# Performance work log

Hardware: AMD Instinct MI355X
Metric: run time of the kernel (lower is better)

Reference implementation:

```python
import jax, jax.numpy as jnp
import numpy as np

DIM = 128
NUM_LAYERS = 2
N_LEGO = 50000
N_POINT = 100000
E_LL = 500000
E_PP = 400000
E_LP = 500000
E_PL = 500000


def _seg_softmax(score, seg, n):
    m = jax.ops.segment_max(score, seg, num_segments=n)
    m = jnp.where(jnp.isfinite(m), m, 0.0)
    e = jnp.exp(score - m[seg])
    d = jax.ops.segment_sum(e, seg, num_segments=n)
    return e / (d[seg] + 1e-16)


def _trans_conv(xs, xd, src, dst, Wq, bq, Wk, bk, Wv, bv, Ws, bs):
    # PyG TransformerConv, heads=1, root skip, no edge features
    q = xd @ Wq + bq
    k = xs @ Wk + bk
    v = xs @ Wv + bv
    score = (q[dst] * k[src]).sum(-1) / jnp.sqrt(jnp.asarray(DIM, q.dtype))
    a = _seg_softmax(score, dst, xd.shape[0])
    agg = jax.ops.segment_sum(a[:, None] * v[src], dst, num_segments=xd.shape[0])
    return agg + xd @ Ws + bs


def _gat_conv(xs, xd, src, dst, W, a_src, a_dst, b):
    # PyG GATConv, heads=1, add_self_loops=False, shared lin for src/dst
    hs = xs @ W
    hd = xd @ W
    score = jax.nn.leaky_relu((hs @ a_src)[src] + (hd @ a_dst)[dst], 0.2)
    a = _seg_softmax(score, dst, xd.shape[0])
    return jax.ops.segment_sum(a[:, None] * hs[src], dst, num_segments=xd.shape[0]) + b


def _edge_conv(x, src, dst, W1, b1, W2, b2):
    # PyG EdgeConv: max_j MLP([x_i, x_j - x_i]); BN treated as identity (eval)
    xi = x[dst]
    h = jax.nn.relu(jnp.concatenate([xi, x[src] - xi], axis=-1) @ W1 + b1)
    m = h @ W2 + b2
    agg = jax.ops.segment_max(m, dst, num_segments=x.shape[0])
    return jnp.where(jnp.isfinite(agg), agg, 0.0)


def _forward(x_lego, x_point, tWq, tbq, tWk, tbk, tWv, tbv, tWs, tbs,
             eW1, eb1, eW2, eb2, gW, gAs, gAd, gb,
             ll_src, ll_dst, pp_src, pp_dst, lp_src, lp_dst, pl_src, pl_dst):
    for layer in range(NUM_LAYERS):
        iA = 2 * layer        # first HeteroConv in the stack
        iB = 2 * layer + 1    # second HeteroConv
        i_lp = 2 * layer      # GAT lego->point instance
        i_pl = 2 * layer + 1  # GAT point->lego instance
        # conv A: 4 relations, HeteroConv sum-aggregation per dst type
        lego_a = _trans_conv(x_lego, x_lego, ll_src, ll_dst,
                             tWq[iA], tbq[iA], tWk[iA], tbk[iA], tWv[iA], tbv[iA], tWs[iA], tbs[iA]) \
               + _gat_conv(x_point, x_lego, pl_src, pl_dst, gW[i_pl], gAs[i_pl], gAd[i_pl], gb[i_pl])
        point_a = _edge_conv(x_point, pp_src, pp_dst, eW1[iA], eb1[iA], eW2[iA], eb2[iA]) \
                + _gat_conv(x_lego, x_point, lp_src, lp_dst, gW[i_lp], gAs[i_lp], gAd[i_lp], gb[i_lp])
        # conv B: intra-type relations only
        x_lego = _trans_conv(lego_a, lego_a, ll_src, ll_dst,
                             tWq[iB], tbq[iB], tWk[iB], tbk[iB], tWv[iB], tbv[iB], tWs[iB], tbs[iB])
        x_point = _edge_conv(point_a, pp_src, pp_dst, eW1[iB], eb1[iB], eW2[iB], eb2[iB])
    return x_lego, x_point


def setup_inputs() -> dict:
    key = jax.random.key(0)
    ks = jax.random.split(key, 32)
    NT = 2 * NUM_LAYERS  # conv instances per conv type
    s = np.float32(1.0 / np.sqrt(DIM))
    sh = np.float32(1.0 / np.sqrt(4 * DIM))
    return {
        "x_lego": jax.random.normal(ks[0], (N_LEGO, DIM), jnp.float32),
        "x_point": jax.random.normal(ks[1], (N_POINT, DIM), jnp.float32),
        "tWq": jax.random.normal(ks[2], (NT, DIM, DIM), jnp.float32) * s,
        "tbq": jnp.zeros((NT, DIM), jnp.float32),
        "tWk": jax.random.normal(ks[3], (NT, DIM, DIM), jnp.float32) * s,
        "tbk": jnp.zeros((NT, DIM), jnp.float32),
        "tWv": jax.random.normal(ks[4], (NT, DIM, DIM), jnp.float32) * s,
        "tbv": jnp.zeros((NT, DIM), jnp.float32),
        "tWs": jax.random.normal(ks[5], (NT, DIM, DIM), jnp.float32) * s,
        "tbs": jnp.zeros((NT, DIM), jnp.float32),
        "eW1": jax.random.normal(ks[6], (NT, 2 * DIM, 4 * DIM), jnp.float32) * s,
        "eb1": jnp.zeros((NT, 4 * DIM), jnp.float32),
        "eW2": jax.random.normal(ks[7], (NT, 4 * DIM, DIM), jnp.float32) * sh,
        "eb2": jnp.zeros((NT, DIM), jnp.float32),
        "gW": jax.random.normal(ks[8], (NT, DIM, DIM), jnp.float32) * s,
        "gAs": jax.random.normal(ks[9], (NT, DIM), jnp.float32) * s,
        "gAd": jax.random.normal(ks[10], (NT, DIM), jnp.float32) * s,
        "gb": jnp.zeros((NT, DIM), jnp.float32),
        "ll_src": jax.random.randint(ks[11], (E_LL,), 0, N_LEGO),
        "ll_dst": jax.random.randint(ks[12], (E_LL,), 0, N_LEGO),
        "pp_src": jax.random.randint(ks[13], (E_PP,), 0, N_POINT),
        "pp_dst": jax.random.randint(ks[14], (E_PP,), 0, N_POINT),
        "lp_src": jax.random.randint(ks[15], (E_LP,), 0, N_LEGO),
        "lp_dst": jax.random.randint(ks[16], (E_LP,), 0, N_POINT),
        "pl_src": jax.random.randint(ks[17], (E_PL,), 0, N_POINT),
        "pl_dst": jax.random.randint(ks[18], (E_PL,), 0, N_LEGO),
    }


def reference(x_lego, x_point, tWq, tbq, tWk, tbk, tWv, tbv, tWs, tbs,
              eW1, eb1, eW2, eb2, gW, gAs, gAd, gb,
              ll_src, ll_dst, pp_src, pp_dst, lp_src, lp_dst, pl_src, pl_dst):
    return _forward(x_lego, x_point, tWq, tbq, tWk, tbk, tWv, tbv, tWs, tbs,
                    eW1, eb1, eW2, eb2, gW, gAs, gAd, gb,
                    ll_src, ll_dst, pp_src, pp_dst, lp_src, lp_dst, pl_src, pl_dst)
```

## Files before the change

### kernel.cpp

```cpp
#include <hip/hip_runtime.h>


typedef unsigned int u32;
typedef unsigned short u16;

#define NL 50000
#define NP 100000
#define ELL 500000
#define EPPE 400000
#define ELPE 500000
#define EPLE 500000
#define ENC_NEG_INF 0x007FFFFFu

using bf16x8 = __attribute__((ext_vector_type(8))) short;
using f32x4  = __attribute__((ext_vector_type(4))) float;
using u16x4  = __attribute__((ext_vector_type(4))) unsigned short;

__device__ __forceinline__ float bf2f(u16 h) { return __uint_as_float(((u32)h) << 16); }
__device__ __forceinline__ u16 f2bf(float f) {
    u32 u = __float_as_uint(f);
    u += 0x7FFFu + ((u >> 16) & 1u);
    return (u16)(u >> 16);
}
__device__ __forceinline__ u32 encf(float f) {
    u32 u = __float_as_uint(f);
    return (u & 0x80000000u) ? ~u : (u | 0x80000000u);
}
__device__ __forceinline__ float decf(u32 u) {
    return __uint_as_float((u & 0x80000000u) ? (u ^ 0x80000000u) : ~u);
}

__global__ void k_detect(const u32* __restrict__ x, u32* __restrict__ flag) {
    int lane = threadIdx.x;
    u16 lo = (u16)(x[lane] & 0xFFFFu);
    float a = fabsf(bf2f(lo));
    int inband = (a > 1e-4f && a < 100.f) ? 1 : 0;
    unsigned long long m = __ballot(inband);
    if (lane == 0) flag[0] = (__popcll(m) >= 32) ? 1u : 0u;
}


__global__ __launch_bounds__(256) void k_cast_any(const void* __restrict__ in,
                                                  float* __restrict__ out, int n,
                                                  const u32* __restrict__ flag) {
    int i = blockIdx.x * 256 + threadIdx.x;
    if (i >= n) return;
    if (flag[0]) out[i] = bf2f(((const u16*)in)[i]);
    else         out[i] = ((const float*)in)[i];
}

__global__ __launch_bounds__(256) void k_store_out(const float* __restrict__ in,
                                                   void* __restrict__ out, size_t off, int n,
                                                   const u32* __restrict__ flag) {
    int i = blockIdx.x * 256 + threadIdx.x;
    if (i >= n) return;
    if (flag[0]) ((u16*)out)[off + i] = f2bf(in[i]);
    else         ((float*)out)[off + i] = in[i];
}

__global__ __launch_bounds__(256) void k_fill_u32(u32* __restrict__ p, u32 v, int n) {
    int i = blockIdx.x * 256 + threadIdx.x;
    if (i < n) p[i] = v;
}

__global__ void k_add128(const float* __restrict__ a, const float* __restrict__ b,
                         float* __restrict__ o) {
    int t = threadIdx.x;
    o[t] = a[t] + b[t];
}

__global__ __launch_bounds__(256) void k_tcast(const float* __restrict__ in,
                                               u16* __restrict__ out,
                                               int K, int N, int total) {
    int i = blockIdx.x * 256 + threadIdx.x;
    if (i >= total) return;
    int per = K * N;
    int c = i / per, r = i - c * per;
    int k = r / N, n = r - k * N;
    out[(size_t)c * per + (size_t)n * K + k] = f2bf(in[i]);
}

__global__ __launch_bounds__(256) void k_w1mod(float* __restrict__ w, int total) {
    int i = blockIdx.x * 256 + threadIdx.x;
    if (i >= total) return;
    int c = i >> 16;
    int r = (i >> 9) & 127;
    int col = i & 511;
    float* base = w + c * 131072;
    base[r * 512 + col] -= base[(r + 128) * 512 + col];
}

__global__ __launch_bounds__(256) void k_split(const float4* __restrict__ x,
                                               u16x4* __restrict__ xh,
                                               u16x4* __restrict__ xl, int n4) {
    int i = blockIdx.x * 256 + threadIdx.x;
    if (i >= n4) return;
    float4 f = x[i];
    float fv[4] = {f.x, f.y, f.z, f.w};
    u16x4 h, l;
#pragma unroll
    for (int j = 0; j < 4; ++j) {
        u16 hi = f2bf(fv[j]);
        h[j] = hi;
        l[j] = f2bf(fv[j] - bf2f(hi));
    }
    xh[i] = h; xl[i] = l;
}

__global__ void k_matvec2(const float* __restrict__ W, const float* __restrict__ a0,
                          const float* __restrict__ a1, float* __restrict__ o) {
    __shared__ float as[128];
    const float* a = blockIdx.x ? a1 : a0;
    int t = threadIdx.x;
    as[t] = a[t];
    __syncthreads();
    float s = 0.f;
#pragma unroll 8
    for (int i = 0; i < 128; ++i) s += W[t * 128 + i] * as[i];
    o[blockIdx.x * 128 + t] = s;
}

__global__ __launch_bounds__(256) void k_node_scalar(const float* __restrict__ X,
                                                     const float* __restrict__ wv,
                                                     float* __restrict__ s, int n) {
    int wid = (blockIdx.x * 256 + threadIdx.x) >> 6;
    int lane = threadIdx.x & 63;
    if (wid >= n) return;
    const float* xr = X + (size_t)wid * 128;
    float v = xr[lane] * wv[lane] + xr[lane + 64] * wv[lane + 64];
#pragma unroll
    for (int o = 32; o; o >>= 1) v += __shfl_xor(v, o);
    if (lane == 0) s[wid] = v;
}


__global__ __launch_bounds__(256) void k_deg(const int* __restrict__ dst,
                                             int* __restrict__ deg, int E) {
    int i = blockIdx.x * 256 + threadIdx.x;
    if (i < E) atomicAdd(deg + dst[i], 1);
}

__global__ __launch_bounds__(256) void k_scan1(const int* __restrict__ deg,
                                               int* __restrict__ rp,
                                               int* __restrict__ aux, int n) {
    __shared__ int ls[256];
    int t = threadIdx.x;
    int i = blockIdx.x * 256 + t;
    int v = (i < n) ? deg[i] : 0;
    ls[t] = v;
    __syncthreads();
#pragma unroll
    for (int off = 1; off < 256; off <<= 1) {
        int a = (t >= off) ? ls[t - off] : 0;
        __syncthreads();
        ls[t] += a;
        __syncthreads();
    }
    if (i < n) rp[i] = ls[t] - v;
    if (t == 255) aux[blockIdx.x] = ls[255];
}

__global__ __launch_bounds__(512) void k_scan2(int* __restrict__ aux, int nb) {
    __shared__ int ls[512];
    int t = threadIdx.x;
    int v = (t < nb) ? aux[t] : 0;
    ls[t] = v;
    __syncthreads();
#pragma unroll
    for (int off = 1; off < 512; off <<= 1) {
        int a = (t >= off) ? ls[t - off] : 0;
        __syncthreads();
        ls[t] += a;
        __syncthreads();
    }
    if (t < nb) aux[t] = ls[t] - v;
}

__global__ __launch_bounds__(256) void k_scan3(int* __restrict__ rp,
                                               const int* __restrict__ aux,
                                               int n, int E) {
    int i = blockIdx.x * 256 + threadIdx.x;
    if (i > n) return;
    if (i == n) rp[n] = E;
    else        rp[i] += aux[i >> 8];
}

__global__ __launch_bounds__(256) void k_copy_i32(const int* __restrict__ a,
                                                  int* __restrict__ b, int n) {
    int i = blockIdx.x * 256 + threadIdx.x;
    if (i < n) b[i] = a[i];
}

__global__ __launch_bounds__(256) void k_scat(const int* __restrict__ src,
                                              const int* __restrict__ dst,
                                              int* __restrict__ cur,
                                              int* __restrict__ col, int E) {
    int i = blockIdx.x * 256 + threadIdx.x;
    if (i >= E) return;
    int pos = atomicAdd(cur + dst[i], 1);
    col[pos] = src[i];
}


__global__ __launch_bounds__(256) void k_attn_trans(const float* __restrict__ Tq,
                                                    const float* __restrict__ Tk,
                                                    const float* __restrict__ Tv,
                                                    const int* __restrict__ rp,
                                                    const int* __restrict__ col,
                                                    float* __restrict__ out, int nd) {
    int row = (blockIdx.x * 256 + threadIdx.x) >> 6;
    int lane = threadIdx.x & 63;
    if (row >= nd) return;
    int e0 = rp[row], e1 = rp[row + 1];
    if (e0 >= e1) return;
    const float* q = Tq + (size_t)row * 128;
    float q0 = q[lane], q1 = q[lane + 64];
    float m = -3.0e38f, l = 0.f, o0 = 0.f, o1 = 0.f;
    for (int e = e0; e < e1; ++e) {
        int s = col[e];
        const float* kr = Tk + (size_t)s * 128;
        float d = q0 * kr[lane] + q1 * kr[lane + 64];
#pragma unroll
        for (int off = 32; off; off >>= 1) d += __shfl_xor(d, off);
        d *= 0.08838834764831845f;
        float mn = fmaxf(m, d);
        float al = expf(m - mn);
        float p  = expf(d - mn);
        const float* vr = Tv + (size_t)s * 128;
        l  = l * al + p;
        o0 = o0 * al + p * vr[lane];
        o1 = o1 * al + p * vr[lane + 64];
        m = mn;
    }
    float inv = 1.f / (l + 1e-16f);
    size_t base = (size_t)row * 128;
    out[base + lane]      += o0 * inv;
    out[base + lane + 64] += o1 * inv;
}

__global__ __launch_bounds__(256) void k_attn_gat(const float* __restrict__ hs,
                                                  const float* __restrict__ ss,
                                                  const float* __restrict__ sd,
                                                  const int* __restrict__ rp,
                                                  const int* __restrict__ col,
                                                  float* __restrict__ out, int nd) {
    int row = (blockIdx.x * 256 + threadIdx.x) >> 6;
    int lane = threadIdx.x & 63;
    if (row >= nd) return;
    int e0 = rp[row], e1 = rp[row + 1];
    if (e0 >= e1) return;
    float sdv = sd[row];
    float m = -3.0e38f, l = 0.f, o0 = 0.f, o1 = 0.f;
    for (int e = e0; e < e1; ++e) {
        int s = col[e];
        float sc = ss[s] + sdv;
        sc = sc > 0.f ? sc : 0.2f * sc;
        float mn = fmaxf(m, sc);
        float al = expf(m - mn);
        float p  = expf(sc - mn);
        const float* hr = hs + (size_t)s * 128;
        l  = l * al + p;
        o0 = o0 * al + p * hr[lane];
        o1 = o1 * al + p * hr[lane + 64];
        m = mn;
    }
    float inv = 1.f / (l + 1e-16f);
    size_t base = (size_t)row * 128;
    out[base + lane]      += o0 * inv;
    out[base + lane + 64] += o1 * inv;
}

#define LSTR 40

__global__ __launch_bounds__(256) void k_mgemm(const float* __restrict__ A_,
                                               const u16* __restrict__ Wt,
                                               const float* __restrict__ bias,
                                               float* __restrict__ Cout,
                                               int M, int N, int K) {
    __shared__ u16 Ahs[128 * LSTR];
    __shared__ u16 Als[128 * LSTR];
    __shared__ u16 Bss[128 * LSTR];
    const int tid = threadIdx.x;
    const int m0 = blockIdx.y * 128, n0 = blockIdx.x * 128;

    const int srow = tid >> 1, sseg = (tid & 1) * 16;
    int arow = m0 + srow;
    if (arow >= M) arow = M - 1;
    const float* Af = A_ + (size_t)arow * K + sseg;
    u16* AhW = &Ahs[srow * LSTR + sseg];
    u16* AlW = &Als[srow * LSTR + sseg];
    const u16* Bp = Wt + (size_t)(n0 + srow) * K + sseg;
    u16* BsW = &Bss[srow * LSTR + sseg];

    const int lane = tid & 63, wv = tid >> 6;
    const int mw = (wv >> 1) * 64, nw = (wv & 1) * 64;
    const int fm = lane & 15, fq = lane >> 4;
    const u16* aRh = &Ahs[(mw + fm) * LSTR + fq * 8];
    const u16* aRl = &Als[(mw + fm) * LSTR + fq * 8];
    const u16* bR  = &Bss[(nw + fm) * LSTR + fq * 8];

    f32x4 acc[4][4];
#pragma unroll
    for (int i = 0; i < 4; ++i)
#pragma unroll
        for (int j = 0; j < 4; ++j) { acc[i][j][0]=0.f; acc[i][j][1]=0.f; acc[i][j][2]=0.f; acc[i][j][3]=0.f; }

    for (int k0 = 0; k0 < K; k0 += 32) {
        __syncthreads();
        float4 f0 = *(const float4*)(Af + k0);
        float4 f1 = *(const float4*)(Af + k0 + 4);
        float4 f2 = *(const float4*)(Af + k0 + 8);
        float4 f3 = *(const float4*)(Af + k0 + 12);
        float v[16] = {f0.x,f0.y,f0.z,f0.w, f1.x,f1.y,f1.z,f1.w,
                       f2.x,f2.y,f2.z,f2.w, f3.x,f3.y,f3.z,f3.w};
        u32 hp[8], lp[8];
#pragma unroll
        for (int i = 0; i < 8; ++i) {
            float x0 = v[2 * i], x1 = v[2 * i + 1];
            u16 h0 = f2bf(x0), h1 = f2bf(x1);
            u16 l0 = f2bf(x0 - bf2f(h0)), l1 = f2bf(x1 - bf2f(h1));
            hp[i] = (u32)h0 | ((u32)h1 << 16);
            lp[i] = (u32)l0 | ((u32)l1 << 16);
        }
        uint4 h04 = {hp[0], hp[1], hp[2], hp[3]}, h48 = {hp[4], hp[5], hp[6], hp[7]};
        uint4 l04 = {lp[0], lp[1], lp[2], lp[3]}, l48 = {lp[4], lp[5], lp[6], lp[7]};
        *(uint4*)AhW = h04; *(uint4*)(AhW + 8) = h48;
        *(uint4*)AlW = l04; *(uint4*)(AlW + 8) = l48;
        *(uint4*)BsW       = *(const uint4*)(Bp + k0);
        *(uint4*)(BsW + 8) = *(const uint4*)(Bp + k0 + 8);
        __syncthreads();

        bf16x8 ah[4], al[4], bfr[4];
#pragma unroll
        for (int i = 0; i < 4; ++i) ah[i]  = *(const bf16x8*)(aRh + i * 16 * LSTR);
#pragma unroll
        for (int i = 0; i < 4; ++i) al[i]  = *(const bf16x8*)(aRl + i * 16 * LSTR);
#pragma unroll
        for (int j = 0; j < 4; ++j) bfr[j] = *(const bf16x8*)(bR + j * 16 * LSTR);
#pragma unroll
        for (int i = 0; i < 4; ++i)
#pragma unroll
            for (int j = 0; j < 4; ++j) {
                acc[i][j] = __builtin_amdgcn_mfma_f32_16x16x32_bf16(ah[i], bfr[j],
                                                                    acc[i][j], 0, 0, 0);
                acc[i][j] = __builtin_amdgcn_mfma_f32_16x16x32_bf16(al[i], bfr[j],
                                                                    acc[i][j], 0, 0, 0);
            }
    }

    float bb[4];
#pragma unroll
    for (int j = 0; j < 4; ++j)
        bb[j] = bias ? bias[n0 + nw + j * 16 + fm] : 0.f;
#pragma unroll
    for (int i = 0; i < 4; ++i) {
#pragma unroll
        for (int reg = 0; reg < 4; ++reg) {
            int r = m0 + mw + i * 16 + fq * 4 + reg;
            if (r >= M) continue;
#pragma unroll
            for (int j = 0; j < 4; ++j)
                Cout[(size_t)r * N + n0 + nw + j * 16 + fm] = acc[i][j][reg] + bb[j];
        }
    }
}

#define LSTRH 72

__global__ __launch_bounds__(256) void k_edge_fused(const u16* __restrict__ Xh,
                                                    const u16* __restrict__ Xl,
                                                    const int* __restrict__ esrc,
                                                    const int* __restrict__ edst,
                                                    const u16* __restrict__ W1t,
                                                    const float* __restrict__ b1,
                                                    const u16* __restrict__ W2t,
                                                    u32* __restrict__ agg, int E) {
    __shared__ u16 Hhs[128 * LSTRH];
    __shared__ u16 Hls[128 * LSTRH];
    const int tid = threadIdx.x;
    const int e0 = blockIdx.x * 128;
    const int lane = tid & 63, wv = tid >> 6;
    const int fm = lane & 15, fq = lane >> 4;
    const int mw1 = wv * 32;
    const int mw2 = (wv >> 1) * 64, nw2 = (wv & 1) * 64;

    const u16 *p0h[2], *p0l[2], *p1h[2], *p1l[2];
    {
        int er0 = e0 + mw1 + fm;       if (er0 >= E) er0 = E - 1;
        int er1 = e0 + mw1 + 16 + fm;  if (er1 >= E) er1 = E - 1;
        size_t d0 = (size_t)edst[er0] * 128, s0 = (size_t)esrc[er0] * 128;
        size_t d1 = (size_t)edst[er1] * 128, s1 = (size_t)esrc[er1] * 128;
        p0h[0] = Xh + d0; p0l[0] = Xl + d0; p0h[1] = Xh + s0; p0l[1] = Xl + s0;
        p1h[0] = Xh + d1; p1l[0] = Xl + d1; p1h[1] = Xh + s1; p1l[1] = Xl + s1;
    }

    f32x4 macc[4][4];
#pragma unroll
    for (int i = 0; i < 4; ++i)
#pragma unroll
        for (int j = 0; j < 4; ++j) { macc[i][j][0]=0.f; macc[i][j][1]=0.f; macc[i][j][2]=0.f; macc[i][j][3]=0.f; }

    for (int nc = 0; nc < 8; ++nc) {
        f32x4 hacc[2][4];
#pragma unroll
        for (int i = 0; i < 2; ++i)
#pragma unroll
            for (int j = 0; j < 4; ++j) { hacc[i][j][0]=0.f; hacc[i][j][1]=0.f; hacc[i][j][2]=0.f; hacc[i][j][3]=0.f; }

        const u16* wbase = W1t + (size_t)(nc * 64 + fm) * 256 + fq * 8;

        auto s1step = [&](const u16* a0h, const u16* a0l, const u16* a1h,
                          const u16* a1l, int kw, int ka) {
            bf16x8 ah0 = *(const bf16x8*)(a0h + ka);
            bf16x8 al0 = *(const bf16x8*)(a0l + ka);
            bf16x8 ah1 = *(const bf16x8*)(a1h + ka);
            bf16x8 al1 = *(const bf16x8*)(a1l + ka);
            bf16x8 bfr[4];
#pragma unroll
            for (int j = 0; j < 4; ++j)
                bfr[j] = *(const bf16x8*)(wbase + kw + j * 16 * 256);
#pragma unroll
            for (int j = 0; j < 4; ++j) {
                hacc[0][j] = __builtin_amdgcn_mfma_f32_16x16x32_bf16(ah0, bfr[j],
                                                                     hacc[0][j], 0, 0, 0);
                hacc[0][j] = __builtin_amdgcn_mfma_f32_16x16x32_bf16(al0, bfr[j],
                                                                     hacc[0][j], 0, 0, 0);
            }
#pragma unroll
            for (int j = 0; j < 4; ++j) {
                hacc[1][j] = __builtin_amdgcn_mfma_f32_16x16x32_bf16(ah1, bfr[j],
                                                                     hacc[1][j], 0, 0, 0);
                hacc[1][j] = __builtin_amdgcn_mfma_f32_16x16x32_bf16(al1, bfr[j],
                                                                     hacc[1][j], 0, 0, 0);
            }
        };

#pragma unroll 2
        for (int k0 = 0; k0 < 128; k0 += 32)
            s1step(p0h[0], p0l[0], p1h[0], p1l[0], k0, k0 + fq * 8);
#pragma unroll 2
        for (int k0 = 128; k0 < 256; k0 += 32)
            s1step(p0h[1], p0l[1], p1h[1], p1l[1], k0, k0 - 128 + fq * 8);

        __syncthreads();
#pragma unroll
        for (int j = 0; j < 4; ++j) {
            int hk = j * 16 + fm;
            float bb = b1[nc * 64 + hk];
#pragma unroll
            for (int i = 0; i < 2; ++i)
#pragma unroll
                for (int reg = 0; reg < 4; ++reg) {
                    int hr = mw1 + i * 16 + fq * 4 + reg;
                    float h = hacc[i][j][reg] + bb;
                    h = h > 0.f ? h : 0.f;
                    u16 hi = f2bf(h);
                    u16 lo = f2bf(h - bf2f(hi));
                    Hhs[hr * LSTRH + hk] = hi;
                    Hls[hr * LSTRH + hk] = lo;
                }
        }
        __syncthreads();

        const u16* w2base = W2t + (size_t)(nw2 + fm) * 512 + nc * 64 + fq * 8;
#pragma unroll
        for (int k0 = 0; k0 < 64; k0 += 32) {
            bf16x8 ah[4], al[4], bfr[4];
#pragma unroll
            for (int i = 0; i < 4; ++i) {
                int off = (mw2 + i * 16 + fm) * LSTRH + k0 + fq * 8;
                ah[i] = *(const bf16x8*)&Hhs[off];
                al[i] = *(const bf16x8*)&Hls[off];
            }
#pragma unroll
            for (int j = 0; j < 4; ++j)
                bfr[j] = *(const bf16x8*)(w2base + k0 + j * 16 * 512);
#pragma unroll
            for (int i = 0; i < 4; ++i)
#pragma unroll
                for (int j = 0; j < 4; ++j) {
                    macc[i][j] = __builtin_amdgcn_mfma_f32_16x16x32_bf16(ah[i], bfr[j],
                                                                         macc[i][j], 0, 0, 0);
                    macc[i][j] = __builtin_amdgcn_mfma_f32_16x16x32_bf16(al[i], bfr[j],
                                                                         macc[i][j], 0, 0, 0);
                }
        }
    }

#pragma unroll
    for (int i = 0; i < 4; ++i) {
#pragma unroll
        for (int reg = 0; reg < 4; ++reg) {
            int r = mw2 + i * 16 + fq * 4 + reg;
            int e = e0 + r;
            if (e >= E) continue;
            u32* base = agg + (size_t)edst[e] * 128 + nw2;
#pragma unroll
            for (int j = 0; j < 4; ++j)
                atomicMax(base + j * 16 + fm, encf(macc[i][j][reg]));
        }
    }
}

__global__ __launch_bounds__(256) void k_decode(u32* __restrict__ agg,
                                                const float* __restrict__ b2,
                                                const float* __restrict__ gb, int n) {
    int i = blockIdx.x * 256 + threadIdx.x;
    if (i >= n) return;
    int c = i & 127;
    u32 u = agg[i];
    float v = (u == ENC_NEG_INF) ? 0.f : (decf(u) + b2[c]);
    if (gb) v += gb[c];
    ((float*)agg)[i] = v;
}


extern "C" void kernel_launch(void* const* d_in, const int* in_sizes, int n_in,
                              void* d_out, int out_size, void* d_ws, size_t ws_size,
                              hipStream_t stream) {
    (void)in_sizes; (void)out_size;
    if (n_in < 26) return;
    if (ws_size < (size_t)240000000) return;

    const void* in_xl  = d_in[0];
    const void* in_xp  = d_in[1];
    const void* in_tWq = d_in[2];
    const void* in_tbq = d_in[3];
    const void* in_tWk = d_in[4];
    const void* in_tbk = d_in[5];
    const void* in_tWv = d_in[6];
    const void* in_tbv = d_in[7];
    const void* in_tWs = d_in[8];
    const void* in_tbs = d_in[9];
    const void* in_eW1 = d_in[10];
    const void* in_eb1 = d_in[11];
    const void* in_eW2 = d_in[12];
    const void* in_eb2 = d_in[13];
    const void* in_gW  = d_in[14];
    const void* in_gAs = d_in[15];
    const void* in_gAd = d_in[16];
    const void* in_gb  = d_in[17];
    const int* ll_src = (const int*)d_in[18];
    const int* ll_dst = (const int*)d_in[19];
    const int* pp_src = (const int*)d_in[20];
    const int* pp_dst = (const int*)d_in[21];
    const int* lp_src = (const int*)d_in[22];
    const int* lp_dst = (const int*)d_in[23];
    const int* pl_src = (const int*)d_in[24];
    const int* pl_dst = (const int*)d_in[25];

    char* w = (char*)d_ws;
    auto alloc = [&](size_t bytes) -> char* {
        char* p = w;
        w += (bytes + 255) & ~(size_t)255;
        return p;
    };
    float* XL   = (float*)alloc((size_t)NL * 128 * 4);
    float* XP   = (float*)alloc((size_t)NP * 128 * 4);
    float* LA   = (float*)alloc((size_t)NL * 128 * 4);
    float* PA   = (float*)alloc((size_t)NP * 128 * 4);
    float* ssrc = (float*)alloc((size_t)NP * 4);
    float* sdst = (float*)alloc((size_t)NP * 4);
    float* wv2  = (float*)alloc(256 * 4);
    float* comb = (float*)alloc(128 * 4);
    u32*  dflag = (u32*)  alloc(256);
    float* tbqf = (float*)alloc(512 * 4);
    float* tbkf = (float*)alloc(512 * 4);
    float* tbvf = (float*)alloc(512 * 4);
    float* tbsf = (float*)alloc(512 * 4);
    float* eb1f = (float*)alloc(2048 * 4);
    float* eb2f = (float*)alloc(512 * 4);
    float* gWf  = (float*)alloc(65536 * 4);
    float* gAsf = (float*)alloc(512 * 4);
    float* gAdf = (float*)alloc(512 * 4);
    float* gbf  = (float*)alloc(512 * 4);
    u16* tWqt = (u16*)alloc(65536 * 2);
    u16* tWkt = (u16*)alloc(65536 * 2);
    u16* tWvt = (u16*)alloc(65536 * 2);
    u16* tWst = (u16*)alloc(65536 * 2);
    u16* gWt  = (u16*)alloc(65536 * 2);
    u16* eW1t = (u16*)alloc(524288 * 2);
    u16* eW2t = (u16*)alloc(262144 * 2);
    int* rp_ll  = (int*)alloc((NL + 1) * 4);
    int* rp_lp  = (int*)alloc((NP + 1) * 4);
    int* rp_pl  = (int*)alloc((NL + 1) * 4);
    int* col_ll = (int*)alloc((size_t)ELL * 4);
    int* col_lp = (int*)alloc((size_t)ELPE * 4);
    int* col_pl = (int*)alloc((size_t)EPLE * 4);
    char* U = alloc(76800000);
    float* tWqf = (float*)U;
    float* tWkf = tWqf + 65536;
    float* tWvf = tWkf + 65536;
    float* tWsf = tWvf + 65536;
    float* eW1f = tWsf + 65536;
    float* eW2f = eW1f + 524288;
    float* Tq  = (float*)U;
    float* Tk  = Tq + (size_t)NL * 128;
    float* Tv  = Tk + (size_t)NL * 128;
    float* Ghs = (float*)U;
    u16* Xph = (u16*)U;
    u16* Xpl = Xph + (size_t)NP * 128;

    k_detect<<<1, 64, 0, stream>>>((const u32*)in_xl, dflag);

    auto cast = [&](const void* s_, float* d_, int n) {
        k_cast_any<<<(n + 255) / 256, 256, 0, stream>>>(s_, d_, n, dflag);
    };
    auto fillu = [&](void* p, u32 v, int n) {
        k_fill_u32<<<(n + 255) / 256, 256, 0, stream>>>((u32*)p, v, n);
    };
    auto tcast = [&](const float* s_, u16* d_, int K, int N, int nconv) {
        int total = nconv * K * N;
        k_tcast<<<(total + 255) / 256, 256, 0, stream>>>(s_, d_, K, N, total);
    };

    cast(in_xl, XL, NL * 128);
    cast(in_xp, XP, NP * 128);
    cast(in_tWq, tWqf, 65536); cast(in_tbq, tbqf, 512);
    cast(in_tWk, tWkf, 65536); cast(in_tbk, tbkf, 512);
    cast(in_tWv, tWvf, 65536); cast(in_tbv, tbvf, 512);
    cast(in_tWs, tWsf, 65536); cast(in_tbs, tbsf, 512);
    cast(in_eW1, eW1f, 524288); cast(in_eb1, eb1f, 2048);
    cast(in_eW2, eW2f, 262144); cast(in_eb2, eb2f, 512);
    cast(in_gW, gWf, 65536);
    cast(in_gAs, gAsf, 512); cast(in_gAd, gAdf, 512); cast(in_gb, gbf, 512);

    k_w1mod<<<(262144 + 255) / 256, 256, 0, stream>>>(eW1f, 262144);

    tcast(tWqf, tWqt, 128, 128, 4);
    tcast(tWkf, tWkt, 128, 128, 4);
    tcast(tWvf, tWvt, 128, 128, 4);
    tcast(tWsf, tWst, 128, 128, 4);
    tcast(gWf,  gWt,  128, 128, 4);
    tcast(eW1f, eW1t, 256, 512, 4);
    tcast(eW2f, eW2t, 512, 128, 4);

    int* deg = (int*)U;
    int* cur = deg + NP + 64;
    int* aux = cur + NP + 64;
    auto build_csr = [&](const int* src, const int* dst, int E, int nd,
                         int* rp, int* col) {
        int nb = (nd + 255) / 256;
        fillu(deg, 0u, nd);
        k_deg<<<(E + 255) / 256, 256, 0, stream>>>(dst, deg, E);
        k_scan1<<<nb, 256, 0, stream>>>(deg, rp, aux, nd);
        k_scan2<<<1, 512, 0, stream>>>(aux, nb);
        k_scan3<<<(nd + 256) / 256, 256, 0, stream>>>(rp, aux, nd, E);
        k_copy_i32<<<(nd + 255) / 256, 256, 0, stream>>>(rp, cur, nd);
        k_scat<<<(E + 255) / 256, 256, 0, stream>>>(src, dst, cur, col, E);
    };
    build_csr(ll_src, ll_dst, ELL, NL, rp_ll, col_ll);
    build_csr(lp_src, lp_dst, ELPE, NP, rp_lp, col_lp);
    build_csr(pl_src, pl_dst, EPLE, NL, rp_pl, col_pl);

    auto mgemm = [&](const float* A, const u16* Wt, const float* b, float* C,
                     int M, int N, int K) {
        dim3 g(N / 128, (M + 127) / 128);
        k_mgemm<<<g, 256, 0, stream>>>(A, Wt, b, C, M, N, K);
    };

    auto trans_agg = [&](const float* Xin, float* out, int conv) {
        mgemm(Xin, tWqt + conv * 16384, tbqf + conv * 128, Tq, NL, 128, 128);
        mgemm(Xin, tWkt + conv * 16384, tbkf + conv * 128, Tk, NL, 128, 128);
        mgemm(Xin, tWvt + conv * 16384, tbvf + conv * 128, Tv, NL, 128, 128);
        k_attn_trans<<<(NL + 3) / 4, 256, 0, stream>>>(Tq, Tk, Tv, rp_ll, col_ll,
                                                       out, NL);
    };
    auto gat_conv = [&](const float* Xs, int ns, int nd,
                        const float* Xd, const int* rp, const int* col,
                        int g, float* out) {
        k_matvec2<<<2, 128, 0, stream>>>(gWf + g * 16384, gAsf + g * 128,
                                         gAdf + g * 128, wv2);
        k_node_scalar<<<(ns * 64 + 255) / 256, 256, 0, stream>>>(Xs, wv2, ssrc, ns);
        k_node_scalar<<<(nd * 64 + 255) / 256, 256, 0, stream>>>(Xd, wv2 + 128, sdst, nd);
        mgemm(Xs, gWt + g * 16384, nullptr, Ghs, ns, 128, 128);
        k_attn_gat<<<(nd + 3) / 4, 256, 0, stream>>>(Ghs, ssrc, sdst, rp, col,
                                                     out, nd);
    };
    auto edge_conv = [&](const float* Xin, float* Xout, int conv, const float* gbext) {
        k_split<<<(NP * 32 + 255) / 256, 256, 0, stream>>>(
            (const float4*)Xin, (u16x4*)Xph, (u16x4*)Xpl, NP * 32);
        fillu(Xout, ENC_NEG_INF, NP * 128);
        k_edge_fused<<<(EPPE + 127) / 128, 256, 0, stream>>>(
            Xph, Xpl, pp_src, pp_dst,
            eW1t + conv * 131072, eb1f + conv * 512, eW2t + conv * 65536,
            (u32*)Xout, EPPE);
        k_decode<<<(NP * 128 + 255) / 256, 256, 0, stream>>>((u32*)Xout, eb2f + conv * 128,
                                                             gbext, NP * 128);
    };

    for (int layer = 0; layer < 2; ++layer) {
        int cA = 2 * layer, cB = cA + 1;
        int g_lp = 2 * layer, g_pl = 2 * layer + 1;

        k_add128<<<1, 128, 0, stream>>>(tbsf + cA * 128, gbf + g_pl * 128, comb);
        mgemm(XL, tWst + cA * 16384, comb, LA, NL, 128, 128);
        trans_agg(XL, LA, cA);
        gat_conv(XP, NP, NL, XL, rp_pl, col_pl, g_pl, LA);

        edge_conv(XP, PA, cA, gbf + g_lp * 128);
        gat_conv(XL, NL, NP, XP, rp_lp, col_lp, g_lp, PA);

        mgemm(LA, tWst + cB * 16384, tbsf + cB * 128, XL, NL, 128, 128);
        trans_agg(LA, XL, cB);
        edge_conv(PA, XP, cB, nullptr);
    }

    k_store_out<<<(NL * 128 + 255) / 256, 256, 0, stream>>>(XL, d_out, 0, NL * 128, dflag);
    k_store_out<<<(NP * 128 + 255) / 256, 256, 0, stream>>>(XP, d_out, (size_t)NL * 128,
                                                            NP * 128, dflag);
}
```

Measured before the change: 5.578 ms.

## Restructure EdgeConv kernel into wave-private 16-edge tiles with register-resident features

The fused EdgeConv kernel is reorganised so each wavefront owns 16 edges end to end. Their gathered destination and source features are loaded into registers once, instead of being re-gathered from global memory for each of the 8 hidden chunks. The first GEMM swaps operand roles so the hidden tile lands per-edge and can go into wave-private shared memory. That removes the block-wide __syncthreads in favour of a local waitcnt, with blocks shrunk to 64 edges and launch bounds set for two blocks per CU. The trade-off is that each wave now streams the full W1/W2 weights for only 16 edges, which raises weight traffic through the caches, and register pressure goes up from holding the features.

After: 6.533 ms. +17.1%, slower.

```diff
diff --git a/kernel.cpp b/kernel.cpp
--- a/kernel.cpp
+++ b/kernel.cpp
@@ -365,140 +365,109 @@
     }
 }
 
-#define LSTRH 72
-
-__global__ __launch_bounds__(256) void k_edge_fused(const u16* __restrict__ Xh,
-                                                    const u16* __restrict__ Xl,
-                                                    const int* __restrict__ esrc,
-                                                    const int* __restrict__ edst,
-                                                    const u16* __restrict__ W1t,
-                                                    const float* __restrict__ b1,
-                                                    const u16* __restrict__ W2t,
-                                                    u32* __restrict__ agg, int E) {
-    __shared__ u16 Hhs[128 * LSTRH];
-    __shared__ u16 Hls[128 * LSTRH];
+#define HST 72
+
+__global__ __launch_bounds__(256, 2) void k_edge_fused(const u16* __restrict__ Xh,
+                                                       const u16* __restrict__ Xl,
+                                                       const int* __restrict__ esrc,
+                                                       const int* __restrict__ edst,
+                                                       const u16* __restrict__ W1t,
+                                                       const float* __restrict__ b1,
+                                                       const u16* __restrict__ W2t,
+                                                       u32* __restrict__ agg, int E) {
+    __shared__ u16 Hh[4 * 16 * HST];
+    __shared__ u16 Hl[4 * 16 * HST];
     const int tid = threadIdx.x;
-    const int e0 = blockIdx.x * 128;
     const int lane = tid & 63, wv = tid >> 6;
     const int fm = lane & 15, fq = lane >> 4;
-    const int mw1 = wv * 32;
-    const int mw2 = (wv >> 1) * 64, nw2 = (wv & 1) * 64;
-
-    const u16 *p0h[2], *p0l[2], *p1h[2], *p1l[2];
-    {
-        int er0 = e0 + mw1 + fm;       if (er0 >= E) er0 = E - 1;
-        int er1 = e0 + mw1 + 16 + fm;  if (er1 >= E) er1 = E - 1;
-        size_t d0 = (size_t)edst[er0] * 128, s0 = (size_t)esrc[er0] * 128;
-        size_t d1 = (size_t)edst[er1] * 128, s1 = (size_t)esrc[er1] * 128;
-        p0h[0] = Xh + d0; p0l[0] = Xl + d0; p0h[1] = Xh + s0; p0l[1] = Xl + s0;
-        p1h[0] = Xh + d1; p1l[0] = Xl + d1; p1h[1] = Xh + s1; p1l[1] = Xl + s1;
-    }
-
-    f32x4 macc[4][4];
-#pragma unroll
-    for (int i = 0; i < 4; ++i)
-#pragma unroll
-        for (int j = 0; j < 4; ++j) { macc[i][j][0]=0.f; macc[i][j][1]=0.f; macc[i][j][2]=0.f; macc[i][j][3]=0.f; }
+    const int e0 = blockIdx.x * 64;
+
+    int eo = e0 + wv * 16 + fm;
+    if (eo >= E) eo = E - 1;
+    const size_t ndof = (size_t)edst[eo] * 128, nsof = (size_t)esrc[eo] * 128;
+
+    bf16x8 xdh[4], xdl[4], xsh[4], xsl[4];
+#pragma unroll
+    for (int t = 0; t < 4; ++t) {
+        int c = t * 32 + fq * 8;
+        xdh[t] = *(const bf16x8*)(Xh + ndof + c);
+        xdl[t] = *(const bf16x8*)(Xl + ndof + c);
+        xsh[t] = *(const bf16x8*)(Xh + nsof + c);
+        xsl[t] = *(const bf16x8*)(Xl + nsof + c);
+    }
+
+    int erow[4];
+#pragma unroll
+    for (int r = 0; r < 4; ++r) {
+        int e = e0 + wv * 16 + fq * 4 + r;
+        erow[r] = (e < E) ? edst[e] : -1;
+    }
+
+    f32x4 macc[8];
+#pragma unroll
+    for (int of = 0; of < 8; ++of) { macc[of][0]=0.f; macc[of][1]=0.f; macc[of][2]=0.f; macc[of][3]=0.f; }
+
+    const int lbase = (wv * 16 + fm) * HST;
 
     for (int nc = 0; nc < 8; ++nc) {
-        f32x4 hacc[2][4];
-#pragma unroll
-        for (int i = 0; i < 2; ++i)
-#pragma unroll
-            for (int j = 0; j < 4; ++j) { hacc[i][j][0]=0.f; hacc[i][j][1]=0.f; hacc[i][j][2]=0.f; hacc[i][j][3]=0.f; }
-
-        const u16* wbase = W1t + (size_t)(nc * 64 + fm) * 256 + fq * 8;
-
-        auto s1step = [&](const u16* a0h, const u16* a0l, const u16* a1h,
-                          const u16* a1l, int kw, int ka) {
-            bf16x8 ah0 = *(const bf16x8*)(a0h + ka);
-            bf16x8 al0 = *(const bf16x8*)(a0l + ka);
-            bf16x8 ah1 = *(const bf16x8*)(a1h + ka);
-            bf16x8 al1 = *(const bf16x8*)(a1l + ka);
-            bf16x8 bfr[4];
-#pragma unroll
-            for (int j = 0; j < 4; ++j)
-                bfr[j] = *(const bf16x8*)(wbase + kw + j * 16 * 256);
-#pragma unroll
-            for (int j = 0; j < 4; ++j) {
-                hacc[0][j] = __builtin_amdgcn_mfma_f32_16x16x32_bf16(ah0, bfr[j],
-                                                                     hacc[0][j], 0, 0, 0);
-                hacc[0][j] = __builtin_amdgcn_mfma_f32_16x16x32_bf16(al0, bfr[j],
-                                                                     hacc[0][j], 0, 0, 0);
+        f32x4 hacc[4];
+#pragma unroll
+        for (int i = 0; i < 4; ++i) { hacc[i][0]=0.f; hacc[i][1]=0.f; hacc[i][2]=0.f; hacc[i][3]=0.f; }
+
+        const u16* w1p = W1t + (size_t)(nc * 64 + fm) * 256 + fq * 8;
+#pragma unroll
+        for (int t = 0; t < 8; ++t) {
+            bf16x8 xh = (t < 4) ? xdh[t] : xsh[t - 4];
+            bf16x8 xl = (t < 4) ? xdl[t] : xsl[t - 4];
+#pragma unroll
+            for (int i = 0; i < 4; ++i) {
+                bf16x8 w1 = *(const bf16x8*)(w1p + (size_t)i * 16 * 256 + t * 32);
+                hacc[i] = __builtin_amdgcn_mfma_f32_16x16x32_bf16(w1, xh, hacc[i], 0, 0, 0);
+                hacc[i] = __builtin_amdgcn_mfma_f32_16x16x32_bf16(w1, xl, hacc[i], 0, 0, 0);
             }
-#pragma unroll
-            for (int j = 0; j < 4; ++j) {
-                hacc[1][j] = __builtin_amdgcn_mfma_f32_16x16x32_bf16(ah1, bfr[j],
-                                                                     hacc[1][j], 0, 0, 0);
-                hacc[1][j] = __builtin_amdgcn_mfma_f32_16x16x32_bf16(al1, bfr[j],
-                                                                     hacc[1][j], 0, 0, 0);
+        }
+
+        asm volatile("s_waitcnt lgkmcnt(0)" ::: "memory");
+#pragma unroll
+        for (int i = 0; i < 4; ++i) {
+            float4 bb = *(const float4*)(b1 + nc * 64 + i * 16 + fq * 4);
+            const float bv[4] = {bb.x, bb.y, bb.z, bb.w};
+            u16 hi[4], lo[4];
+#pragma unroll
+            for (int r = 0; r < 4; ++r) {
+                float h = hacc[i][r] + bv[r];
+                h = h > 0.f ? h : 0.f;
+                hi[r] = f2bf(h);
+                lo[r] = f2bf(h - bf2f(hi[r]));
             }
-        };
-
-#pragma unroll 2
-        for (int k0 = 0; k0 < 128; k0 += 32)
-            s1step(p0h[0], p0l[0], p1h[0], p1l[0], k0, k0 + fq * 8);
-#pragma unroll 2
-        for (int k0 = 128; k0 < 256; k0 += 32)
-            s1step(p0h[1], p0l[1], p1h[1], p1l[1], k0, k0 - 128 + fq * 8);
-
-        __syncthreads();
-#pragma unroll
-        for (int j = 0; j < 4; ++j) {
-            int hk = j * 16 + fm;
-            float bb = b1[nc * 64 + hk];
-#pragma unroll
-            for (int i = 0; i < 2; ++i)
-#pragma unroll
-                for (int reg = 0; reg < 4; ++reg) {
-                    int hr = mw1 + i * 16 + fq * 4 + reg;
-                    float h = hacc[i][j][reg] + bb;
-                    h = h > 0.f ? h : 0.f;
-                    u16 hi = f2bf(h);
-                    u16 lo = f2bf(h - bf2f(hi));
-                    Hhs[hr * LSTRH + hk] = hi;
-                    Hls[hr * LSTRH + hk] = lo;
-                }
+            uint2 ph = {(u32)hi[0] | ((u32)hi[1] << 16), (u32)hi[2] | ((u32)hi[3] << 16)};
+            uint2 pl = {(u32)lo[0] | ((u32)lo[1] << 16), (u32)lo[2] | ((u32)lo[3] << 16)};
+            *(uint2*)&Hh[lbase + i * 16 + fq * 4] = ph;
+            *(uint2*)&Hl[lbase + i * 16 + fq * 4] = pl;
         }
-        __syncthreads();
-
-        const u16* w2base = W2t + (size_t)(nw2 + fm) * 512 + nc * 64 + fq * 8;
-#pragma unroll
-        for (int k0 = 0; k0 < 64; k0 += 32) {
-            bf16x8 ah[4], al[4], bfr[4];
-#pragma unroll
-            for (int i = 0; i < 4; ++i) {
-                int off = (mw2 + i * 16 + fm) * LSTRH + k0 + fq * 8;
-                ah[i] = *(const bf16x8*)&Hhs[off];
-                al[i] = *(const bf16x8*)&Hls[off];
+        asm volatile("s_waitcnt lgkmcnt(0)" ::: "memory");
+
+#pragma unroll
+        for (int kk = 0; kk < 2; ++kk) {
+            bf16x8 ah = *(const bf16x8*)&Hh[lbase + kk * 32 + fq * 8];
+            bf16x8 al = *(const bf16x8*)&Hl[lbase + kk * 32 + fq * 8];
+            const u16* w2p = W2t + (size_t)fm * 512 + nc * 64 + kk * 32 + fq * 8;
+#pragma unroll
+            for (int of = 0; of < 8; ++of) {
+                bf16x8 w2 = *(const bf16x8*)(w2p + (size_t)of * 16 * 512);
+                macc[of] = __builtin_amdgcn_mfma_f32_16x16x32_bf16(ah, w2, macc[of], 0, 0, 0);
+                macc[of] = __builtin_amdgcn_mfma_f32_16x16x32_bf16(al, w2, macc[of], 0, 0, 0);
             }
-#pragma unroll
-            for (int j = 0; j < 4; ++j)
-                bfr[j] = *(const bf16x8*)(w2base + k0 + j * 16 * 512);
-#pragma unroll
-            for (int i = 0; i < 4; ++i)
-#pragma unroll
-                for (int j = 0; j < 4; ++j) {
-                    macc[i][j] = __builtin_amdgcn_mfma_f32_16x16x32_bf16(ah[i], bfr[j],
-                                                                         macc[i][j], 0, 0, 0);
-                    macc[i][j] = __builtin_amdgcn_mfma_f32_16x16x32_bf16(al[i], bfr[j],
-                                                                         macc[i][j], 0, 0, 0);
-                }
         }
     }
 
 #pragma unroll
-    for (int i = 0; i < 4; ++i) {
-#pragma unroll
-        for (int reg = 0; reg < 4; ++reg) {
-            int r = mw2 + i * 16 + fq * 4 + reg;
-            int e = e0 + r;
-            if (e >= E) continue;
-            u32* base = agg + (size_t)edst[e] * 128 + nw2;
-#pragma unroll
-            for (int j = 0; j < 4; ++j)
-                atomicMax(base + j * 16 + fm, encf(macc[i][j][reg]));
-        }
+    for (int r = 0; r < 4; ++r) {
+        if (erow[r] < 0) continue;
+        u32* base = agg + (size_t)erow[r] * 128 + fm;
+#pragma unroll
+        for (int of = 0; of < 8; ++of)
+            atomicMax(base + of * 16, encf(macc[of][r]));
     }
 }
 
@@ -681,7 +650,7 @@
         k_split<<<(NP * 32 + 255) / 256, 256, 0, stream>>>(
             (const float4*)Xin, (u16x4*)Xph, (u16x4*)Xpl, NP * 32);
         fillu(Xout, ENC_NEG_INF, NP * 128);
-        k_edge_fused<<<(EPPE + 127) / 128, 256, 0, stream>>>(
+        k_edge_fused<<<(EPPE + 63) / 64, 256, 0, stream>>>(
             Xph, Xpl, pp_src, pp_dst,
             eW1t + conv * 131072, eb1f + conv * 512, eW2t + conv * 65536,
             (u32*)Xout, EPPE);
```
